# Performance work log

Hardware: AMD Instinct MI355X
Metric: run time of the kernel (lower is better)

The kernel has to match this reference:

```python
import jax, jax.numpy as jnp
import numpy as np

B, T, S, L, D, H = 2, 1024, 8, 256, 1024, 16
DH = D // H
EPS = 1e-5


def layer_norm(x, w, b):
    m = jnp.mean(x, axis=-1, keepdims=True)
    v = jnp.mean(jnp.square(x - m), axis=-1, keepdims=True)
    return (x - m) * jax.lax.rsqrt(v + EPS) * w + b


def setup_inputs() -> dict:
    key = jax.random.key(0)
    ks = jax.random.split(key, 12)
    s = 0.02
    return {
        "target_hidden": jax.random.normal(ks[0], (B, T, D), jnp.float32),
        "support_hidden": jax.random.normal(ks[1], (B, S, L, D), jnp.float32),
        "support_features": jax.random.normal(ks[2], (B, T, 3), jnp.float32),
        "support_token_mask": jax.random.randint(ks[3], (B, S, L), 0, 2).astype(bool),
        "ln_q_w": jnp.ones((D,), jnp.float32), "ln_q_b": jnp.zeros((D,), jnp.float32),
        "ln_kv_w": jnp.ones((D,), jnp.float32), "ln_kv_b": jnp.zeros((D,), jnp.float32),
        "out_ln_w": jnp.ones((D,), jnp.float32), "out_ln_b": jnp.zeros((D,), jnp.float32),
        "in_proj_w": jax.random.normal(ks[4], (3 * D, D), jnp.float32) * s,
        "in_proj_b": jnp.zeros((3 * D,), jnp.float32),
        "out_proj_w": jax.random.normal(ks[5], (D, D), jnp.float32) * s,
        "out_proj_b": jnp.zeros((D,), jnp.float32),
        "gate_w1": jax.random.normal(ks[6], (D, 2 * D + 3), jnp.float32) * s,
        "gate_b1": jnp.zeros((D,), jnp.float32),
        "gate_w2": jax.random.normal(ks[7], (1, D), jnp.float32) * s,
        "gate_b2": jnp.zeros((1,), jnp.float32),
    }


def _forward(target_hidden, support_hidden, support_features,
             ln_q_w, ln_q_b, ln_kv_w, ln_kv_b, out_ln_w, out_ln_b,
             in_proj_w, in_proj_b, out_proj_w, out_proj_b,
             gate_w1, gate_b1, gate_w2, gate_b2, support_token_mask):
    b, ns, sl, d = support_hidden.shape
    kv_len = ns * sl
    support_flat = support_hidden.reshape(b, kv_len, d)
    mask_flat = support_token_mask.reshape(b, kv_len)  # True = valid token

    q_in = layer_norm(target_hidden, ln_q_w, ln_q_b)
    kv_in = layer_norm(support_flat, ln_kv_w, ln_kv_b)

    # in-projection (torch MHA packed qkv weight)
    q = q_in @ in_proj_w[:d].T + in_proj_b[:d]
    k = kv_in @ in_proj_w[d:2 * d].T + in_proj_b[d:2 * d]
    v = kv_in @ in_proj_w[2 * d:].T + in_proj_b[2 * d:]

    qh = q.reshape(b, -1, H, DH)
    kh = k.reshape(b, kv_len, H, DH)
    vh = v.reshape(b, kv_len, H, DH)

    scores = jnp.einsum("bthd,bshd->bhts", qh, kh) / jnp.sqrt(jnp.float32(DH))
    scores = jnp.where(mask_flat[:, None, None, :], scores, -jnp.inf)
    probs = jax.nn.softmax(scores, axis=-1)
    ctx = jnp.einsum("bhts,bshd->bthd", probs, vh).reshape(b, -1, d)
    attn_out = ctx @ out_proj_w.T + out_proj_b

    gate_in = jnp.concatenate([target_hidden, attn_out, support_features], axis=-1)
    h = jax.nn.gelu(gate_in @ gate_w1.T + gate_b1, approximate=False)
    gate = jax.nn.sigmoid(h @ gate_w2.T + gate_b2)  # [b, t, 1]

    fused = gate * attn_out + (1.0 - gate) * target_hidden
    out = layer_norm(target_hidden + fused, out_ln_w, out_ln_b)
    return out, gate.squeeze(-1)


def reference(target_hidden, support_hidden, support_features, support_token_mask,
              ln_q_w, ln_q_b, ln_kv_w, ln_kv_b, out_ln_w, out_ln_b,
              in_proj_w, in_proj_b, out_proj_w, out_proj_b,
              gate_w1, gate_b1, gate_w2, gate_b2):
    return _forward(target_hidden, support_hidden, support_features,
                    ln_q_w, ln_q_b, ln_kv_w, ln_kv_b, out_ln_w, out_ln_b,
                    in_proj_w, in_proj_b, out_proj_w, out_proj_b,
                    gate_w1, gate_b1, gate_w2, gate_b2, support_token_mask)
```

## Files before the change

### kernel.cpp

```cpp
#include <hip/hip_runtime.h>
#include <stdint.h>

#define DEV __device__ __forceinline__

typedef __attribute__((ext_vector_type(8))) short bf16x8;
typedef __attribute__((ext_vector_type(4))) float f32x4;
typedef __attribute__((ext_vector_type(16))) float f32x16;
typedef __attribute__((ext_vector_type(8))) unsigned short ushort8;

DEV unsigned short f2bf(float f) {
  unsigned u = __float_as_uint(f);
  return (unsigned short)((u + 0x7fffu + ((u >> 16) & 1u)) >> 16);
}
DEV float bf2f(unsigned short h) { return __uint_as_float(((unsigned)h) << 16); }

DEV unsigned cvtpk(float lo, float hi) {
  unsigned r;
  asm("v_cvt_pk_bf16_f32 %0, %1, %2" : "=v"(r) : "v"(lo), "v"(hi));
  return r;
}
DEV void pl32swap(unsigned& a, unsigned& b) {
  asm volatile("v_permlane32_swap_b32 %0, %1" : "+v"(a), "+v"(b));
}

DEV void async16(const void* g, void* l) {
  __builtin_amdgcn_global_load_lds((const __attribute__((address_space(1))) void*)g,
                                   (__attribute__((address_space(3))) void*)l, 16, 0, 0);
}

__global__ void k_prep(const float4* __restrict__ ipw, const float4* __restrict__ opw,
                       const float* __restrict__ g1w, ushort4* __restrict__ Wbf,
                       ushort4* __restrict__ Wobf, unsigned short* __restrict__ Wg1bf) {
  int bid = blockIdx.x, t = threadIdx.x;
  if (bid < 3072) {
    int i = bid * 256 + t;
    float4 v = ipw[i];
    ushort4 o; o.x = f2bf(v.x); o.y = f2bf(v.y); o.z = f2bf(v.z); o.w = f2bf(v.w);
    Wbf[i] = o;
  } else if (bid < 4096) {
    int i = (bid - 3072) * 256 + t;
    float4 v = opw[i];
    ushort4 o; o.x = f2bf(v.x); o.y = f2bf(v.y); o.z = f2bf(v.z); o.w = f2bf(v.w);
    Wobf[i] = o;
  } else {
    for (int i = (bid - 4096) * 256 + t; i < 1024 * 2080; i += 2048 * 256) {
      int r = i / 2080, c = i - r * 2080;
      Wg1bf[i] = (c < 2051) ? f2bf(g1w[(size_t)r * 2051 + c]) : (unsigned short)0;
    }
  }
}

__global__ void k_mask_build(const unsigned char* __restrict__ m, unsigned short* __restrict__ mf) {
  int any = 0;
  for (int i = threadIdx.x; i < 4096; i += 256)
    if ((i & 3) != 0 && m[i] != 0) any = 1;
  unsigned long long ball = __ballot(any);
  __shared__ int sr[4];
  if ((threadIdx.x & 63) == 0) sr[threadIdx.x >> 6] = (ball != 0ULL) ? 1 : 0;
  __syncthreads();
  int isbool = sr[0] | sr[1] | sr[2] | sr[3];
  int i = blockIdx.x * 256 + threadIdx.x;
  if (i < 4096) {
    int v = isbool ? (m[i] != 0) : (((const int*)m)[i] != 0);
    mf[i] = v ? f2bf(-8.0f) : f2bf(-1e30f);
  }
}

__global__ void k_ln2(const float* __restrict__ tgt, const float* __restrict__ sup,
                      const float* __restrict__ qw, const float* __restrict__ qb,
                      const float* __restrict__ kw, const float* __restrict__ kb,
                      unsigned short* __restrict__ qin, unsigned short* __restrict__ kvin) {
  int row = blockIdx.x;
  const float *x, *w, *bb;
  unsigned short* y;
  if (row < 2048) { x = tgt + (size_t)row * 1024; w = qw; bb = qb; y = qin + (size_t)row * 1024; }
  else { int r = row - 2048; x = sup + (size_t)r * 1024; w = kw; bb = kb; y = kvin + (size_t)r * 1024; }
  float4 v = ((const float4*)x)[threadIdx.x];
  float s = v.x + v.y + v.z + v.w;
  float ss = v.x * v.x + v.y * v.y + v.z * v.z + v.w * v.w;
#pragma unroll
  for (int m = 32; m >= 1; m >>= 1) { s += __shfl_xor(s, m); ss += __shfl_xor(ss, m); }
  __shared__ float red[8];
  int wv = threadIdx.x >> 6;
  if ((threadIdx.x & 63) == 0) { red[wv] = s; red[4 + wv] = ss; }
  __syncthreads();
  s = red[0] + red[1] + red[2] + red[3];
  ss = red[4] + red[5] + red[6] + red[7];
  float mean = s * (1.f / 1024.f);
  float var = ss * (1.f / 1024.f) - mean * mean;
  float inv = rsqrtf(var + 1e-5f);
  float4 wv4 = ((const float4*)w)[threadIdx.x];
  float4 bv4 = ((const float4*)bb)[threadIdx.x];
  ushort4 o;
  o.x = f2bf((v.x - mean) * inv * wv4.x + bv4.x);
  o.y = f2bf((v.y - mean) * inv * wv4.y + bv4.y);
  o.z = f2bf((v.z - mean) * inv * wv4.z + bv4.z);
  o.w = f2bf((v.w - mean) * inv * wv4.w + bv4.w);
  ((ushort4*)y)[threadIdx.x] = o;
}

template <int BM, int BN, int OUTMODE>
DEV void gemm_body(const unsigned short* __restrict__ A, const unsigned short* __restrict__ B,
                   const float* __restrict__ bias, void* __restrict__ Cout, int N, int K,
                   int m0, int n0, float* __restrict__ aux, float oscale) {
  constexpr int WM = BM / 2, WN = BN / 2, FM = WM / 16, FN = WN / 16;
  __shared__ __align__(16) unsigned short As[2][BM * 32];
  __shared__ __align__(16) unsigned short Bs[2][BN * 32];
  int tid = threadIdx.x, l = tid & 63, w = tid >> 6;
  int wm = w >> 1, wn = w & 1;

  f32x4 acc[FM][FN];
#pragma unroll
  for (int m = 0; m < FM; m++)
#pragma unroll
    for (int n = 0; n < FN; n++) acc[m][n] = (f32x4){0.f, 0.f, 0.f, 0.f};

  auto stage = [&](int buf, int k0) {
#pragma unroll
    for (int i = 0; i < BM / 64; i++) {
      int r = i * 64 + w * 16 + (l >> 2);
      int cb = ((l & 3) * 16) ^ (((r >> 1) & 3) << 4);
      async16((const char*)A + (((size_t)(m0 + r) * K + k0) * 2 + cb),
              (char*)&As[buf][0] + (i * 64 + w * 16) * 64);
    }
#pragma unroll
    for (int i = 0; i < BN / 64; i++) {
      int r = i * 64 + w * 16 + (l >> 2);
      int cb = ((l & 3) * 16) ^ (((r >> 1) & 3) << 4);
      async16((const char*)B + (((size_t)(n0 + r) * K + k0) * 2 + cb),
              (char*)&Bs[buf][0] + (i * 64 + w * 16) * 64);
    }
  };

  int nk = K / 32;
  stage(0, 0);
  __syncthreads();
  int cur = 0;
  for (int kt = 0; kt < nk; kt++) {
    if (kt + 1 < nk) stage(cur ^ 1, (kt + 1) * 32);
    bf16x8 af[FM], bfr[FN];
#pragma unroll
    for (int m = 0; m < FM; m++) {
      int rr = wm * WM + m * 16 + (l & 15);
      af[m] = *(const bf16x8*)((const char*)&As[cur][0] + rr * 64 +
                               ((16 * (l >> 4)) ^ (((rr >> 1) & 3) << 4)));
    }
#pragma unroll
    for (int n = 0; n < FN; n++) {
      int rr = wn * WN + n * 16 + (l & 15);
      bfr[n] = *(const bf16x8*)((const char*)&Bs[cur][0] + rr * 64 +
                                ((16 * (l >> 4)) ^ (((rr >> 1) & 3) << 4)));
    }
    __builtin_amdgcn_s_setprio(1);
#pragma unroll
    for (int m = 0; m < FM; m++)
#pragma unroll
      for (int n = 0; n < FN; n++)
        acc[m][n] = __builtin_amdgcn_mfma_f32_16x16x32_bf16(af[m], bfr[n], acc[m][n], 0, 0, 0);
    __builtin_amdgcn_s_setprio(0);
    __syncthreads();
    cur ^= 1;
  }

#pragma unroll
  for (int m = 0; m < FM; m++)
#pragma unroll
    for (int n = 0; n < FN; n++)
#pragma unroll
      for (int r = 0; r < 4; r++) {
        int gr = m0 + wm * WM + m * 16 + (l >> 4) * 4 + r;
        int gc = n0 + wn * WN + n * 16 + (l & 15);
        float v = (acc[m][n][r] + bias[gc]) * oscale;
        if (OUTMODE == 2) v = 0.5f * v * (1.f + erff(v * 0.70710678118f));
        if (OUTMODE == 3) {
          aux[(size_t)gr * 1024 + gc] = v;
          ((unsigned short*)Cout)[(size_t)gr * 2080 + 1024 + gc] = f2bf(v);
        } else {
          ((unsigned short*)Cout)[(size_t)gr * N + gc] = f2bf(v);
        }
      }
}

template <int BM, int BN, int OUTMODE>
__global__ __launch_bounds__(256, 2)
void k_gemm(const unsigned short* __restrict__ A, const unsigned short* __restrict__ B,
            const float* __restrict__ bias, void* __restrict__ Cout, int N, int K,
            int nx, float* __restrict__ aux) {
  int cpx = gridDim.x >> 3;
  int orig = (blockIdx.x & 7) * cpx + (blockIdx.x >> 3);
  int m0 = (orig / nx) * BM, n0 = (orig % nx) * BN;
  gemm_body<BM, BN, OUTMODE>(A, B, bias, Cout, N, K, m0, n0, aux, 1.0f);
}

__global__ __launch_bounds__(256, 2)
void k_inproj(const unsigned short* __restrict__ qin, const unsigned short* __restrict__ kvin,
              const unsigned short* __restrict__ Wbf, const float* __restrict__ ipb,
              unsigned short* __restrict__ qbuf, unsigned short* __restrict__ kvbuf) {
  int cpx = gridDim.x >> 3;
  int orig = (blockIdx.x & 7) * cpx + (blockIdx.x >> 3);
  if (orig < 128) {
    int m0 = (orig >> 3) * 128, n0 = (orig & 7) * 128;
    gemm_body<128, 128, 0>(qin, Wbf, ipb, qbuf, 1024, 1024, m0, n0, nullptr, 0.125f);
  } else {
    int t = orig - 128;
    int m0 = (t >> 4) * 128, n0 = (t & 15) * 128;
    gemm_body<128, 128, 0>(kvin, Wbf + 1024 * 1024, ipb + 1024, kvbuf, 2048, 1024, m0, n0,
                           nullptr, 1.0f);
  }
}

__global__ void k_transpose_v(const unsigned short* __restrict__ kvb,
                              unsigned short* __restrict__ vt) {
  __shared__ unsigned short t[64][66];
  int kv0 = blockIdx.x * 64, d0 = blockIdx.y * 64, b = blockIdx.z;
  for (int i = threadIdx.x; i < 4096; i += 256) {
    int r = i >> 6, c = i & 63;
    t[r][c] = kvb[(size_t)(b * 2048 + kv0 + r) * 2048 + 1024 + d0 + c];
  }
  __syncthreads();
  for (int i = threadIdx.x; i < 4096; i += 256) {
    int r = i >> 6, c = i & 63;
    vt[(size_t)(b * 1024 + d0 + r) * 2048 + kv0 + c] = t[c][r];
  }
}

__global__ __launch_bounds__(256, 2)
void k_attn(const unsigned short* __restrict__ qb, const unsigned short* __restrict__ kvb,
            const unsigned short* __restrict__ vt, const unsigned short* __restrict__ maskbf,
            unsigned short* __restrict__ pot, float* __restrict__ plsum) {
  __shared__ __align__(16) unsigned short Kt[2][32 * 64];
  __shared__ __align__(16) unsigned short Vt[2][64 * 32];
  __shared__ __align__(16) unsigned short mls[512];
  int tid = threadIdx.x, l = tid & 63, w = tid >> 6;
  int hi = l >> 5, q32 = l & 31;
  int id = blockIdx.x;
  int hb = id & 31, rest = id >> 5;
  int qt = rest >> 2, seg = rest & 3;
  int h = hb & 15, b = hb >> 4;
  int qrow = qt * 128 + w * 32 + q32;
  int kv0base = seg * 512;

  bf16x8 fq[4];
  const char* qsrc = (const char*)qb + (((size_t)(b * 1024 + qrow)) * 1024 + h * 64 + hi * 8) * 2;
#pragma unroll
  for (int i = 0; i < 4; i++) fq[i] = *(const bf16x8*)(qsrc + i * 32);

  bf16x8 onesB = {0, 0, 0, 0, 0, 0, 0, 0};
  if (hi == 0) onesB[0] = (short)0x3F80;

  f32x16 oa0 = {0, 0, 0, 0, 0, 0, 0, 0, 0, 0, 0, 0, 0, 0, 0, 0};
  f32x16 oa1 = {0, 0, 0, 0, 0, 0, 0, 0, 0, 0, 0, 0, 0, 0, 0, 0};
  float plocal = 0.f;

  if (w == 0)
    async16((const char*)maskbf + ((size_t)b * 2048 + kv0base) * 2 + l * 16, (char*)mls);

  const char* kgb = (const char*)kvb + ((size_t)(b * 2048)) * 4096 + h * 128;
  const char* vgb = (const char*)vt + ((size_t)(b * 1024 + h * 64)) * 4096;
  int kcb = (((l & 7) ^ ((l >> 3) & 7)) << 4);
  int vcb = (((l & 3) ^ ((l >> 3) & 3)) << 4);

  auto stage = [&](int buf, int kv0) {
    async16(kgb + (size_t)(kv0 + w * 8 + (l >> 3)) * 4096 + kcb, (char*)&Kt[buf][0] + w * 1024);
    async16(vgb + (size_t)(w * 16 + (l >> 2)) * 4096 + (size_t)kv0 * 2 + vcb,
            (char*)&Vt[buf][0] + w * 1024);
  };

  stage(0, kv0base);
  __syncthreads();
  int cur = 0;

  int kfs = q32 & 7;
  int vfs = (q32 >> 1) & 3;

  for (int t = 0; t < 16; t++) {
    int kv0 = kv0base + t * 32;
    if (t < 15) stage(cur ^ 1, kv0 + 32);

    f32x16 sac = {0, 0, 0, 0, 0, 0, 0, 0, 0, 0, 0, 0, 0, 0, 0, 0};
    const char* kt = (const char*)&Kt[cur][0];
    __builtin_amdgcn_s_setprio(1);
#pragma unroll
    for (int i = 0; i < 4; i++) {
      bf16x8 ka = *(const bf16x8*)(kt + q32 * 128 + (((i * 2 + hi) ^ kfs) << 4));
      sac = __builtin_amdgcn_mfma_f32_32x32x16_bf16(ka, fq[i], sac, 0, 0, 0);
    }
    unsigned short mv = mls[t * 32 + q32];
    bf16x8 ma = {0, 0, 0, 0, 0, 0, 0, 0};
    if (hi == 0) ma[0] = (short)mv;
    sac = __builtin_amdgcn_mfma_f32_32x32x16_bf16(ma, onesB, sac, 0, 0, 0);
    __builtin_amdgcn_s_setprio(0);

    float p[16];
#pragma unroll
    for (int j = 0; j < 16; j++) p[j] = __expf(sac[j]);
#pragma unroll
    for (int j = 0; j < 16; j++) plocal += p[j];

    bf16x8 pf[2];
#pragma unroll
    for (int c = 0; c < 2; c++) {
      unsigned A0 = cvtpk(p[c * 8 + 0], p[c * 8 + 1]);
      unsigned A1 = cvtpk(p[c * 8 + 2], p[c * 8 + 3]);
      unsigned B0 = cvtpk(p[c * 8 + 4], p[c * 8 + 5]);
      unsigned B1 = cvtpk(p[c * 8 + 6], p[c * 8 + 7]);
      pl32swap(A0, B0);
      pl32swap(A1, B1);
      unsigned fr[4] = {A0, A1, B0, B1};
      pf[c] = *(const bf16x8*)fr;
    }

    const char* vtb = (const char*)&Vt[cur][0];
    __builtin_amdgcn_s_setprio(1);
#pragma unroll
    for (int c = 0; c < 2; c++) {
      bf16x8 va0 = *(const bf16x8*)(vtb + q32 * 64 + (((c * 2 + hi) ^ vfs) << 4));
      bf16x8 va1 = *(const bf16x8*)(vtb + (32 + q32) * 64 + (((c * 2 + hi) ^ vfs) << 4));
      oa0 = __builtin_amdgcn_mfma_f32_32x32x16_bf16(va0, pf[c], oa0, 0, 0, 0);
      oa1 = __builtin_amdgcn_mfma_f32_32x32x16_bf16(va1, pf[c], oa1, 0, 0, 0);
    }
    __builtin_amdgcn_s_setprio(0);
    __syncthreads();
    cur ^= 1;
  }

  float ptot = plocal + __shfl_xor(plocal, 32);
  if (hi == 0) plsum[((size_t)seg * 2048 + b * 1024 + qrow) * 16 + h] = ptot;

  size_t pb = (((size_t)seg * 2 + b) * 16 + h) * 64;
#pragma unroll
  for (int j = 0; j < 16; j++) {
    int d0 = (j & 3) + 8 * (j >> 2) + 4 * hi;
    pot[(pb + d0) * 1024 + qrow] = f2bf(oa0[j]);
    pot[(pb + 32 + d0) * 1024 + qrow] = f2bf(oa1[j]);
  }
}

__global__ void k_combine_t(const unsigned short* __restrict__ pot,
                            const float* __restrict__ plsum, unsigned short* __restrict__ ctx) {
  __shared__ float sinv[64];
  __shared__ __align__(16) unsigned short tl[64][72];
  int t = threadIdx.x;
  int id = blockIdx.x;
  int qt2 = id & 15, bh = id >> 4, h = bh & 15, b = bh >> 4;
  int q0 = qt2 * 64;

  if (t < 64) {
    float s = 0.f;
#pragma unroll
    for (int seg = 0; seg < 4; seg++)
      s += plsum[((size_t)seg * 2048 + b * 1024 + q0 + t) * 16 + h];
    sinv[t] = 1.f / s;
  }

  int d = t >> 2, qo = (t & 3) * 16;
  float acc[16];
#pragma unroll
  for (int j = 0; j < 16; j++) acc[j] = 0.f;
#pragma unroll
  for (int seg = 0; seg < 4; seg++) {
    size_t base = ((((size_t)seg * 2 + b) * 16 + h) * 64 + d) * 1024 + q0 + qo;
    ushort8 v0 = *(const ushort8*)(pot + base);
    ushort8 v1 = *(const ushort8*)(pot + base + 8);
#pragma unroll
    for (int j = 0; j < 8; j++) { acc[j] += bf2f(v0[j]); acc[8 + j] += bf2f(v1[j]); }
  }
  __syncthreads();
#pragma unroll
  for (int j = 0; j < 16; j++) tl[qo + j][d] = f2bf(acc[j] * sinv[qo + j]);
  __syncthreads();

  int q = t >> 2, dof = (t & 3) * 16;
  ushort8 a = *(const ushort8*)&tl[q][dof];
  ushort8 c8 = *(const ushort8*)&tl[q][dof + 8];
  size_t ob = ((size_t)(b * 1024 + q0 + q)) * 1024 + h * 64 + dof;
  *(ushort8*)(ctx + ob) = a;
  *(ushort8*)(ctx + ob + 8) = c8;
}

__global__ void k_gin_static(const float* __restrict__ target, const float* __restrict__ feats,
                             unsigned short* __restrict__ gi) {
  int i = blockIdx.x * 256 + threadIdx.x;
  const int ntgt = 2048 * 1024;
  if (i < ntgt) {
    int r = i >> 10, c = i & 1023;
    gi[(size_t)r * 2080 + c] = f2bf(target[i]);
  } else {
    int j = i - ntgt;
    if (j < 2048 * 32) {
      int r = j >> 5, c = j & 31;
      gi[(size_t)r * 2080 + 2048 + c] = (c < 3) ? f2bf(feats[r * 3 + c]) : (unsigned short)0;
    }
  }
}

__global__ void k_gatefinal(const unsigned short* __restrict__ hm, const float* __restrict__ w2,
                            const float* __restrict__ b2, const float* __restrict__ target,
                            const float* __restrict__ attn, const float* __restrict__ w,
                            const float* __restrict__ bb, float* __restrict__ out,
                            float* __restrict__ gout) {
  int row = blockIdx.x;
  float4 w2v = ((const float4*)w2)[threadIdx.x];
  ushort4 hv = ((const ushort4*)(hm + (size_t)row * 1024))[threadIdx.x];
  float s = bf2f(hv.x) * w2v.x + bf2f(hv.y) * w2v.y + bf2f(hv.z) * w2v.z + bf2f(hv.w) * w2v.w;
#pragma unroll
  for (int m = 32; m >= 1; m >>= 1) s += __shfl_xor(s, m);
  __shared__ float red[8];
  __shared__ float gsh;
  if ((threadIdx.x & 63) == 0) red[threadIdx.x >> 6] = s;
  __syncthreads();
  if (threadIdx.x == 0) {
    float tt = red[0] + red[1] + red[2] + red[3] + b2[0];
    float gv = 1.f / (1.f + __expf(-tt));
    gsh = gv;
    gout[row] = gv;
  }
  __syncthreads();
  float gv = gsh;

  float4 t = ((const float4*)(target + (size_t)row * 1024))[threadIdx.x];
  float4 a = ((const float4*)(attn + (size_t)row * 1024))[threadIdx.x];
  float4 y;
  y.x = (2.f - gv) * t.x + gv * a.x;
  y.y = (2.f - gv) * t.y + gv * a.y;
  y.z = (2.f - gv) * t.z + gv * a.z;
  y.w = (2.f - gv) * t.w + gv * a.w;
  float sm = y.x + y.y + y.z + y.w;
  float ss = y.x * y.x + y.y * y.y + y.z * y.z + y.w * y.w;
#pragma unroll
  for (int m = 32; m >= 1; m >>= 1) { sm += __shfl_xor(sm, m); ss += __shfl_xor(ss, m); }
  if ((threadIdx.x & 63) == 0) { red[threadIdx.x >> 6] = sm; red[4 + (threadIdx.x >> 6)] = ss; }
  __syncthreads();
  sm = red[0] + red[1] + red[2] + red[3];
  ss = red[4] + red[5] + red[6] + red[7];
  float mean = sm * (1.f / 1024.f);
  float var = ss * (1.f / 1024.f) - mean * mean;
  float inv = rsqrtf(var + 1e-5f);
  float4 wv4 = ((const float4*)w)[threadIdx.x];
  float4 bv4 = ((const float4*)bb)[threadIdx.x];
  float4 o;
  o.x = (y.x - mean) * inv * wv4.x + bv4.x;
  o.y = (y.y - mean) * inv * wv4.y + bv4.y;
  o.z = (y.z - mean) * inv * wv4.z + bv4.z;
  o.w = (y.w - mean) * inv * wv4.w + bv4.w;
  ((float4*)(out + (size_t)row * 1024))[threadIdx.x] = o;
}

extern "C" void kernel_launch(void* const* d_in, const int* in_sizes, int n_in,
                              void* d_out, int out_size, void* d_ws, size_t ws_size,
                              hipStream_t stream) {
  const float* target     = (const float*)d_in[0];
  const float* support    = (const float*)d_in[1];
  const float* feats      = (const float*)d_in[2];
  const void*  maskp      = d_in[3];
  const float* ln_q_w     = (const float*)d_in[4];
  const float* ln_q_b     = (const float*)d_in[5];
  const float* ln_kv_w    = (const float*)d_in[6];
  const float* ln_kv_b    = (const float*)d_in[7];
  const float* out_ln_w   = (const float*)d_in[8];
  const float* out_ln_b   = (const float*)d_in[9];
  const float* in_proj_w  = (const float*)d_in[10];
  const float* in_proj_b  = (const float*)d_in[11];
  const float* out_proj_w = (const float*)d_in[12];
  const float* out_proj_b = (const float*)d_in[13];
  const float* gate_w1    = (const float*)d_in[14];
  const float* gate_b1    = (const float*)d_in[15];
  const float* gate_w2    = (const float*)d_in[16];
  const float* gate_b2    = (const float*)d_in[17];

  if (ws_size < 84615168ULL) return;

  char* ws = (char*)d_ws;
  unsigned short* Wbf    = (unsigned short*)(ws + 0);
  unsigned short* Wobf   = (unsigned short*)(ws + 6291456);
  unsigned short* Wg1bf  = (unsigned short*)(ws + 8388608);
  unsigned short* qin    = (unsigned short*)(ws + 12648448);
  unsigned short* kvin   = (unsigned short*)(ws + 16842752);
  unsigned short* qbuf   = (unsigned short*)(ws + 25231360);
  unsigned short* kvbuf  = (unsigned short*)(ws + 29425664);
  unsigned short* vtbuf  = (unsigned short*)(ws + 12648448);
  unsigned short* hbuf   = (unsigned short*)(ws + 25231360);
  unsigned short* ctx    = (unsigned short*)(ws + 46202880);
  float*          attn   = (float*)(ws + 50397184);
  unsigned short* gin    = (unsigned short*)(ws + 58785792);
  unsigned short* pot    = (unsigned short*)(ws + 67305472);
  float*          plsum  = (float*)(ws + 84082688);
  unsigned short* maskbf = (unsigned short*)(ws + 84606976);

  float* outp = (float*)d_out;

  k_mask_build<<<16, 256, 0, stream>>>((const unsigned char*)maskp, maskbf);
  k_prep<<<6144, 256, 0, stream>>>((const float4*)in_proj_w, (const float4*)out_proj_w,
                                   gate_w1, (ushort4*)Wbf, (ushort4*)Wobf, Wg1bf);
  k_gin_static<<<(2048 * 1056 + 255) / 256, 256, 0, stream>>>(target, feats, gin);
  k_ln2<<<6144, 256, 0, stream>>>(target, support, ln_q_w, ln_q_b, ln_kv_w, ln_kv_b, qin, kvin);

  k_inproj<<<640, 256, 0, stream>>>(qin, kvin, Wbf, in_proj_b, qbuf, kvbuf);
  k_transpose_v<<<dim3(32, 16, 2), 256, 0, stream>>>(kvbuf, vtbuf);

  k_attn<<<1024, 256, 0, stream>>>(qbuf, kvbuf, vtbuf, maskbf, pot, plsum);
  k_combine_t<<<512, 256, 0, stream>>>(pot, plsum, ctx);

  k_gemm<64, 64, 3><<<512, 256, 0, stream>>>(ctx, Wobf, out_proj_b, gin, 1024, 1024, 16, attn);

  k_gemm<64, 64, 2><<<512, 256, 0, stream>>>(gin, Wg1bf, gate_b1, hbuf, 1024, 2080, 16, nullptr);

  k_gatefinal<<<2048, 256, 0, stream>>>(hbuf, gate_w2, gate_b2, target, attn,
                                        out_ln_w, out_ln_b, outp, outp + 2 * 1024 * 1024);
}
```

Measured before the change: 265.9 us.

## Fold out-projection into gate weights and merge prep launches into one kernel

The attention branch of the gate's first layer is rewritten algebraically. The gate weights for that branch are pre-multiplied by the transposed out-projection weights, giving a matrix F and a folded bias, so one post-attention GEMM against [Wo; F] produces both attn_out and its gate contribution. The target/features part of the gate GEMM and the F product move into the in-projection launch, and the separate mask, prep, gin and layernorm kernels are merged into one big prep launch. This is meant to shorten the serial chain after attention and cut launch count. In exchange it adds an extra 1024^3 GEMM per call, a larger workspace, and extra bf16 rounding from computing F in reduced precision.

```diff
diff --git a/kernel.cpp b/kernel.cpp
--- a/kernel.cpp
+++ b/kernel.cpp
@@ -28,84 +28,135 @@
                                    (__attribute__((address_space(3))) void*)l, 16, 0, 0);
 }
 
-__global__ void k_prep(const float4* __restrict__ ipw, const float4* __restrict__ opw,
-                       const float* __restrict__ g1w, ushort4* __restrict__ Wbf,
-                       ushort4* __restrict__ Wobf, unsigned short* __restrict__ Wg1bf) {
+__global__ void k_prep_all(const unsigned char* __restrict__ mask, const float4* __restrict__ ipw,
+                           const float* __restrict__ opw, const float* __restrict__ g1w,
+                           const float* __restrict__ tgt, const float* __restrict__ feats,
+                           const float* __restrict__ sup,
+                           const float* __restrict__ qw, const float* __restrict__ qb,
+                           const float* __restrict__ kw, const float* __restrict__ kb,
+                           const float* __restrict__ bo,
+                           unsigned short* __restrict__ maskbf, ushort4* __restrict__ Wbf,
+                           unsigned short* __restrict__ Wobf, unsigned short* __restrict__ WoT,
+                           unsigned short* __restrict__ Wg1attn, unsigned short* __restrict__ Wg1ab,
+                           unsigned short* __restrict__ tgtfeats, unsigned short* __restrict__ qin,
+                           unsigned short* __restrict__ kvin, float* __restrict__ pbias) {
+  __shared__ unsigned short tl[64][65];
+  __shared__ float red[8];
+  __shared__ int sr[4];
   int bid = blockIdx.x, t = threadIdx.x;
-  if (bid < 3072) {
+  if (bid < 16) {
+    int any = 0;
+    for (int i = t; i < 4096; i += 256)
+      if ((i & 3) != 0 && mask[i] != 0) any = 1;
+    unsigned long long ball = __ballot(any);
+    if ((t & 63) == 0) sr[t >> 6] = (ball != 0ULL) ? 1 : 0;
+    __syncthreads();
+    int isbool = sr[0] | sr[1] | sr[2] | sr[3];
     int i = bid * 256 + t;
+    int v = isbool ? (mask[i] != 0) : (((const int*)mask)[i] != 0);
+    maskbf[i] = v ? f2bf(-8.0f) : f2bf(-1e30f);
+  } else if (bid < 3088) {
+    int i = (bid - 16) * 256 + t;
     float4 v = ipw[i];
     ushort4 o; o.x = f2bf(v.x); o.y = f2bf(v.y); o.z = f2bf(v.z); o.w = f2bf(v.w);
     Wbf[i] = o;
-  } else if (bid < 4096) {
-    int i = (bid - 3072) * 256 + t;
-    float4 v = opw[i];
-    ushort4 o; o.x = f2bf(v.x); o.y = f2bf(v.y); o.z = f2bf(v.z); o.w = f2bf(v.w);
-    Wobf[i] = o;
+  } else if (bid < 3344) {
+    int b2 = bid - 3088;
+    int r0 = (b2 >> 4) * 64, c0 = (b2 & 15) * 64;
+#pragma unroll
+    for (int i = 0; i < 16; i++) {
+      int idx = i * 256 + t, rr = idx >> 6, cc = idx & 63;
+      unsigned short bv = f2bf(opw[(size_t)(r0 + rr) * 1024 + c0 + cc]);
+      Wobf[(size_t)(r0 + rr) * 1024 + c0 + cc] = bv;
+      tl[cc][rr] = bv;
+    }
+    __syncthreads();
+#pragma unroll
+    for (int i = 0; i < 16; i++) {
+      int idx = i * 256 + t, rr = idx & 63, cc = idx >> 6;
+      WoT[(size_t)(c0 + cc) * 1024 + r0 + rr] = tl[cc][rr];
+    }
+  } else if (bid < 4368) {
+    int r = bid - 3344;
+    const float* src = g1w + (size_t)r * 2051 + 1024;
+    int c = t * 4;
+    ushort4 o;
+    o.x = f2bf(src[c]); o.y = f2bf(src[c + 1]); o.z = f2bf(src[c + 2]); o.w = f2bf(src[c + 3]);
+    *(ushort4*)(Wg1attn + (size_t)r * 1024 + c) = o;
+  } else if (bid < 5392) {
+    int r = bid - 4368;
+    const float* src = g1w + (size_t)r * 2051;
+    for (int q = t; q < 264; q += 256) {
+      int c = q * 4;
+      ushort4 o;
+#pragma unroll
+      for (int j = 0; j < 4; j++) {
+        int cs = c + j;
+        float v = (cs < 1024) ? src[cs] : ((cs < 1027) ? src[1024 + cs] : 0.f);
+        ((unsigned short*)&o)[j] = f2bf(v);
+      }
+      *(ushort4*)(Wg1ab + (size_t)r * 1056 + c) = o;
+    }
+  } else if (bid < 7440) {
+    int r = bid - 5392;
+    for (int q = t; q < 264; q += 256) {
+      int c = q * 4;
+      ushort4 o;
+#pragma unroll
+      for (int j = 0; j < 4; j++) {
+        int cs = c + j;
+        float v = (cs < 1024) ? tgt[(size_t)r * 1024 + cs]
+                              : ((cs < 1027) ? feats[r * 3 + cs - 1024] : 0.f);
+        ((unsigned short*)&o)[j] = f2bf(v);
+      }
+      *(ushort4*)(tgtfeats + (size_t)r * 1056 + c) = o;
+    }
+  } else if (bid < 13584) {
+    int row = bid - 7440;
+    const float *x, *w, *bb2;
+    unsigned short* y;
+    if (row < 2048) { x = tgt + (size_t)row * 1024; w = qw; bb2 = qb; y = qin + (size_t)row * 1024; }
+    else { int r = row - 2048; x = sup + (size_t)r * 1024; w = kw; bb2 = kb; y = kvin + (size_t)r * 1024; }
+    float4 v = ((const float4*)x)[t];
+    float s = v.x + v.y + v.z + v.w;
+    float ss = v.x * v.x + v.y * v.y + v.z * v.z + v.w * v.w;
+#pragma unroll
+    for (int m = 32; m >= 1; m >>= 1) { s += __shfl_xor(s, m); ss += __shfl_xor(ss, m); }
+    int wv = t >> 6;
+    if ((t & 63) == 0) { red[wv] = s; red[4 + wv] = ss; }
+    __syncthreads();
+    s = red[0] + red[1] + red[2] + red[3];
+    ss = red[4] + red[5] + red[6] + red[7];
+    float mean = s * (1.f / 1024.f);
+    float var = ss * (1.f / 1024.f) - mean * mean;
+    float inv = rsqrtf(var + 1e-5f);
+    float4 wv4 = ((const float4*)w)[t];
+    float4 bv4 = ((const float4*)bb2)[t];
+    ushort4 o;
+    o.x = f2bf((v.x - mean) * inv * wv4.x + bv4.x);
+    o.y = f2bf((v.y - mean) * inv * wv4.y + bv4.y);
+    o.z = f2bf((v.z - mean) * inv * wv4.z + bv4.z);
+    o.w = f2bf((v.w - mean) * inv * wv4.w + bv4.w);
+    ((ushort4*)y)[t] = o;
+  } else if (bid < 13648) {
+    int b7 = bid - 13584;
+    int n = b7 * 16 + (t >> 4), l16 = t & 15;
+    const float* wrow = g1w + (size_t)n * 2051 + 1024;
+    float s = 0.f;
+    for (int j = 0; j < 64; j++) s += bo[l16 + 16 * j] * wrow[l16 + 16 * j];
+#pragma unroll
+    for (int m = 1; m < 16; m <<= 1) s += __shfl_xor(s, m);
+    if (l16 == 0) pbias[1024 + n] = s;
   } else {
-    for (int i = (bid - 4096) * 256 + t; i < 1024 * 2080; i += 2048 * 256) {
-      int r = i / 2080, c = i - r * 2080;
-      Wg1bf[i] = (c < 2051) ? f2bf(g1w[(size_t)r * 2051 + c]) : (unsigned short)0;
-    }
-  }
-}
-
-__global__ void k_mask_build(const unsigned char* __restrict__ m, unsigned short* __restrict__ mf) {
-  int any = 0;
-  for (int i = threadIdx.x; i < 4096; i += 256)
-    if ((i & 3) != 0 && m[i] != 0) any = 1;
-  unsigned long long ball = __ballot(any);
-  __shared__ int sr[4];
-  if ((threadIdx.x & 63) == 0) sr[threadIdx.x >> 6] = (ball != 0ULL) ? 1 : 0;
-  __syncthreads();
-  int isbool = sr[0] | sr[1] | sr[2] | sr[3];
-  int i = blockIdx.x * 256 + threadIdx.x;
-  if (i < 4096) {
-    int v = isbool ? (m[i] != 0) : (((const int*)m)[i] != 0);
-    mf[i] = v ? f2bf(-8.0f) : f2bf(-1e30f);
-  }
-}
-
-__global__ void k_ln2(const float* __restrict__ tgt, const float* __restrict__ sup,
-                      const float* __restrict__ qw, const float* __restrict__ qb,
-                      const float* __restrict__ kw, const float* __restrict__ kb,
-                      unsigned short* __restrict__ qin, unsigned short* __restrict__ kvin) {
-  int row = blockIdx.x;
-  const float *x, *w, *bb;
-  unsigned short* y;
-  if (row < 2048) { x = tgt + (size_t)row * 1024; w = qw; bb = qb; y = qin + (size_t)row * 1024; }
-  else { int r = row - 2048; x = sup + (size_t)r * 1024; w = kw; bb = kb; y = kvin + (size_t)r * 1024; }
-  float4 v = ((const float4*)x)[threadIdx.x];
-  float s = v.x + v.y + v.z + v.w;
-  float ss = v.x * v.x + v.y * v.y + v.z * v.z + v.w * v.w;
-#pragma unroll
-  for (int m = 32; m >= 1; m >>= 1) { s += __shfl_xor(s, m); ss += __shfl_xor(ss, m); }
-  __shared__ float red[8];
-  int wv = threadIdx.x >> 6;
-  if ((threadIdx.x & 63) == 0) { red[wv] = s; red[4 + wv] = ss; }
-  __syncthreads();
-  s = red[0] + red[1] + red[2] + red[3];
-  ss = red[4] + red[5] + red[6] + red[7];
-  float mean = s * (1.f / 1024.f);
-  float var = ss * (1.f / 1024.f) - mean * mean;
-  float inv = rsqrtf(var + 1e-5f);
-  float4 wv4 = ((const float4*)w)[threadIdx.x];
-  float4 bv4 = ((const float4*)bb)[threadIdx.x];
-  ushort4 o;
-  o.x = f2bf((v.x - mean) * inv * wv4.x + bv4.x);
-  o.y = f2bf((v.y - mean) * inv * wv4.y + bv4.y);
-  o.z = f2bf((v.z - mean) * inv * wv4.z + bv4.z);
-  o.w = f2bf((v.w - mean) * inv * wv4.w + bv4.w);
-  ((ushort4*)y)[threadIdx.x] = o;
+    ((float4*)pbias)[t] = ((const float4*)bo)[t];
+  }
 }
 
 template <int BM, int BN, int OUTMODE>
 DEV void gemm_body(const unsigned short* __restrict__ A, const unsigned short* __restrict__ B,
                    const float* __restrict__ bias, void* __restrict__ Cout, int N, int K,
-                   int m0, int n0, float* __restrict__ aux, float oscale) {
+                   int m0, int n0, float oscale, unsigned short* As, unsigned short* Bs) {
   constexpr int WM = BM / 2, WN = BN / 2, FM = WM / 16, FN = WN / 16;
-  __shared__ __align__(16) unsigned short As[2][BM * 32];
-  __shared__ __align__(16) unsigned short Bs[2][BN * 32];
   int tid = threadIdx.x, l = tid & 63, w = tid >> 6;
   int wm = w >> 1, wn = w & 1;
 
@@ -121,14 +172,14 @@
       int r = i * 64 + w * 16 + (l >> 2);
       int cb = ((l & 3) * 16) ^ (((r >> 1) & 3) << 4);
       async16((const char*)A + (((size_t)(m0 + r) * K + k0) * 2 + cb),
-              (char*)&As[buf][0] + (i * 64 + w * 16) * 64);
+              (char*)As + buf * (BM * 64) + (i * 64 + w * 16) * 64);
     }
 #pragma unroll
     for (int i = 0; i < BN / 64; i++) {
       int r = i * 64 + w * 16 + (l >> 2);
       int cb = ((l & 3) * 16) ^ (((r >> 1) & 3) << 4);
       async16((const char*)B + (((size_t)(n0 + r) * K + k0) * 2 + cb),
-              (char*)&Bs[buf][0] + (i * 64 + w * 16) * 64);
+              (char*)Bs + buf * (BN * 64) + (i * 64 + w * 16) * 64);
     }
   };
 
@@ -142,13 +193,13 @@
 #pragma unroll
     for (int m = 0; m < FM; m++) {
       int rr = wm * WM + m * 16 + (l & 15);
-      af[m] = *(const bf16x8*)((const char*)&As[cur][0] + rr * 64 +
+      af[m] = *(const bf16x8*)((const char*)As + cur * (BM * 64) + rr * 64 +
                                ((16 * (l >> 4)) ^ (((rr >> 1) & 3) << 4)));
     }
 #pragma unroll
     for (int n = 0; n < FN; n++) {
       int rr = wn * WN + n * 16 + (l & 15);
-      bfr[n] = *(const bf16x8*)((const char*)&Bs[cur][0] + rr * 64 +
+      bfr[n] = *(const bf16x8*)((const char*)Bs + cur * (BN * 64) + rr * 64 +
                                 ((16 * (l >> 4)) ^ (((rr >> 1) & 3) << 4)));
     }
     __builtin_amdgcn_s_setprio(1);
@@ -170,43 +221,55 @@
       for (int r = 0; r < 4; r++) {
         int gr = m0 + wm * WM + m * 16 + (l >> 4) * 4 + r;
         int gc = n0 + wn * WN + n * 16 + (l & 15);
-        float v = (acc[m][n][r] + bias[gc]) * oscale;
-        if (OUTMODE == 2) v = 0.5f * v * (1.f + erff(v * 0.70710678118f));
-        if (OUTMODE == 3) {
-          aux[(size_t)gr * 1024 + gc] = v;
-          ((unsigned short*)Cout)[(size_t)gr * 2080 + 1024 + gc] = f2bf(v);
-        } else {
+        float v = acc[m][n][r];
+        if (OUTMODE != 4) v += bias[gc];
+        v *= oscale;
+        if (OUTMODE == 1)
+          ((float*)Cout)[(size_t)gr * N + gc] = v;
+        else
           ((unsigned short*)Cout)[(size_t)gr * N + gc] = f2bf(v);
-        }
       }
 }
 
-template <int BM, int BN, int OUTMODE>
 __global__ __launch_bounds__(256, 2)
-void k_gemm(const unsigned short* __restrict__ A, const unsigned short* __restrict__ B,
-            const float* __restrict__ bias, void* __restrict__ Cout, int N, int K,
-            int nx, float* __restrict__ aux) {
-  int cpx = gridDim.x >> 3;
-  int orig = (blockIdx.x & 7) * cpx + (blockIdx.x >> 3);
-  int m0 = (orig / nx) * BM, n0 = (orig % nx) * BN;
-  gemm_body<BM, BN, OUTMODE>(A, B, bias, Cout, N, K, m0, n0, aux, 1.0f);
-}
-
-__global__ __launch_bounds__(256, 2)
-void k_inproj(const unsigned short* __restrict__ qin, const unsigned short* __restrict__ kvin,
-              const unsigned short* __restrict__ Wbf, const float* __restrict__ ipb,
-              unsigned short* __restrict__ qbuf, unsigned short* __restrict__ kvbuf) {
+void k_mm1(const unsigned short* __restrict__ qin, const unsigned short* __restrict__ kvin,
+           const unsigned short* __restrict__ tgtfeats, const unsigned short* __restrict__ Wg1attn,
+           const unsigned short* __restrict__ Wbf, const unsigned short* __restrict__ Wg1ab,
+           const unsigned short* __restrict__ WoT, const float* __restrict__ ipb,
+           const float* __restrict__ g1b, unsigned short* __restrict__ qbuf,
+           unsigned short* __restrict__ kvbuf, float* __restrict__ h1buf,
+           unsigned short* __restrict__ Fbf) {
+  __shared__ __align__(16) unsigned short As[2 * 128 * 32];
+  __shared__ __align__(16) unsigned short Bs[2 * 128 * 32];
   int cpx = gridDim.x >> 3;
   int orig = (blockIdx.x & 7) * cpx + (blockIdx.x >> 3);
   if (orig < 128) {
-    int m0 = (orig >> 3) * 128, n0 = (orig & 7) * 128;
-    gemm_body<128, 128, 0>(qin, Wbf, ipb, qbuf, 1024, 1024, m0, n0, nullptr, 0.125f);
+    gemm_body<128, 128, 0>(qin, Wbf, ipb, qbuf, 1024, 1024, (orig >> 3) * 128, (orig & 7) * 128,
+                           0.125f, As, Bs);
+  } else if (orig < 640) {
+    int t = orig - 128;
+    gemm_body<128, 128, 0>(kvin, Wbf + 1024 * 1024, ipb + 1024, kvbuf, 2048, 1024,
+                           (t >> 4) * 128, (t & 15) * 128, 1.0f, As, Bs);
+  } else if (orig < 768) {
+    int t = orig - 640;
+    gemm_body<128, 128, 1>(tgtfeats, Wg1ab, g1b, h1buf, 1024, 1056, (t >> 3) * 128,
+                           (t & 7) * 128, 1.0f, As, Bs);
   } else {
-    int t = orig - 128;
-    int m0 = (t >> 4) * 128, n0 = (t & 15) * 128;
-    gemm_body<128, 128, 0>(kvin, Wbf + 1024 * 1024, ipb + 1024, kvbuf, 2048, 1024, m0, n0,
-                           nullptr, 1.0f);
-  }
+    int t = orig - 768;
+    gemm_body<64, 64, 4>(Wg1attn, WoT, nullptr, Fbf, 1024, 1024, (t >> 4) * 64, (t & 15) * 64,
+                         1.0f, As, Bs);
+  }
+}
+
+__global__ __launch_bounds__(256, 2)
+void k_mm2(const unsigned short* __restrict__ ctx, const unsigned short* __restrict__ Bw,
+           const float* __restrict__ pbias, float* __restrict__ hc) {
+  __shared__ __align__(16) unsigned short As[2 * 128 * 32];
+  __shared__ __align__(16) unsigned short Bs[2 * 64 * 32];
+  int cpx = gridDim.x >> 3;
+  int orig = (blockIdx.x & 7) * cpx + (blockIdx.x >> 3);
+  gemm_body<128, 64, 1>(ctx, Bw, pbias, hc, 2048, 1024, (orig >> 5) * 128, (orig & 31) * 64,
+                        1.0f, As, Bs);
 }
 
 __global__ void k_transpose_v(const unsigned short* __restrict__ kvb,
@@ -378,38 +441,29 @@
   *(ushort8*)(ctx + ob + 8) = c8;
 }
 
-__global__ void k_gin_static(const float* __restrict__ target, const float* __restrict__ feats,
-                             unsigned short* __restrict__ gi) {
-  int i = blockIdx.x * 256 + threadIdx.x;
-  const int ntgt = 2048 * 1024;
-  if (i < ntgt) {
-    int r = i >> 10, c = i & 1023;
-    gi[(size_t)r * 2080 + c] = f2bf(target[i]);
-  } else {
-    int j = i - ntgt;
-    if (j < 2048 * 32) {
-      int r = j >> 5, c = j & 31;
-      gi[(size_t)r * 2080 + 2048 + c] = (c < 3) ? f2bf(feats[r * 3 + c]) : (unsigned short)0;
-    }
-  }
-}
-
-__global__ void k_gatefinal(const unsigned short* __restrict__ hm, const float* __restrict__ w2,
-                            const float* __restrict__ b2, const float* __restrict__ target,
-                            const float* __restrict__ attn, const float* __restrict__ w,
+__global__ void k_gatefinal(const float* __restrict__ h1, const float* __restrict__ hc,
+                            const float* __restrict__ w2, const float* __restrict__ b2,
+                            const float* __restrict__ target, const float* __restrict__ w,
                             const float* __restrict__ bb, float* __restrict__ out,
                             float* __restrict__ gout) {
-  int row = blockIdx.x;
-  float4 w2v = ((const float4*)w2)[threadIdx.x];
-  ushort4 hv = ((const ushort4*)(hm + (size_t)row * 1024))[threadIdx.x];
-  float s = bf2f(hv.x) * w2v.x + bf2f(hv.y) * w2v.y + bf2f(hv.z) * w2v.z + bf2f(hv.w) * w2v.w;
+  int row = blockIdx.x, t = threadIdx.x;
+  float4 h1v = ((const float4*)(h1 + (size_t)row * 1024))[t];
+  float4 hav = ((const float4*)(hc + (size_t)row * 2048 + 1024))[t];
+  float4 w2v = ((const float4*)w2)[t];
+  float4 g4;
+  g4.x = h1v.x + hav.x; g4.y = h1v.y + hav.y; g4.z = h1v.z + hav.z; g4.w = h1v.w + hav.w;
+  g4.x = 0.5f * g4.x * (1.f + erff(g4.x * 0.70710678118f));
+  g4.y = 0.5f * g4.y * (1.f + erff(g4.y * 0.70710678118f));
+  g4.z = 0.5f * g4.z * (1.f + erff(g4.z * 0.70710678118f));
+  g4.w = 0.5f * g4.w * (1.f + erff(g4.w * 0.70710678118f));
+  float s = g4.x * w2v.x + g4.y * w2v.y + g4.z * w2v.z + g4.w * w2v.w;
 #pragma unroll
   for (int m = 32; m >= 1; m >>= 1) s += __shfl_xor(s, m);
   __shared__ float red[8];
   __shared__ float gsh;
-  if ((threadIdx.x & 63) == 0) red[threadIdx.x >> 6] = s;
-  __syncthreads();
-  if (threadIdx.x == 0) {
+  if ((t & 63) == 0) red[t >> 6] = s;
+  __syncthreads();
+  if (t == 0) {
     float tt = red[0] + red[1] + red[2] + red[3] + b2[0];
     float gv = 1.f / (1.f + __expf(-tt));
     gsh = gv;
@@ -418,32 +472,32 @@
   __syncthreads();
   float gv = gsh;
 
-  float4 t = ((const float4*)(target + (size_t)row * 1024))[threadIdx.x];
-  float4 a = ((const float4*)(attn + (size_t)row * 1024))[threadIdx.x];
+  float4 tg = ((const float4*)(target + (size_t)row * 1024))[t];
+  float4 a = ((const float4*)(hc + (size_t)row * 2048))[t];
   float4 y;
-  y.x = (2.f - gv) * t.x + gv * a.x;
-  y.y = (2.f - gv) * t.y + gv * a.y;
-  y.z = (2.f - gv) * t.z + gv * a.z;
-  y.w = (2.f - gv) * t.w + gv * a.w;
+  y.x = (2.f - gv) * tg.x + gv * a.x;
+  y.y = (2.f - gv) * tg.y + gv * a.y;
+  y.z = (2.f - gv) * tg.z + gv * a.z;
+  y.w = (2.f - gv) * tg.w + gv * a.w;
   float sm = y.x + y.y + y.z + y.w;
   float ss = y.x * y.x + y.y * y.y + y.z * y.z + y.w * y.w;
 #pragma unroll
   for (int m = 32; m >= 1; m >>= 1) { sm += __shfl_xor(sm, m); ss += __shfl_xor(ss, m); }
-  if ((threadIdx.x & 63) == 0) { red[threadIdx.x >> 6] = sm; red[4 + (threadIdx.x >> 6)] = ss; }
+  if ((t & 63) == 0) { red[t >> 6] = sm; red[4 + (t >> 6)] = ss; }
   __syncthreads();
   sm = red[0] + red[1] + red[2] + red[3];
   ss = red[4] + red[5] + red[6] + red[7];
   float mean = sm * (1.f / 1024.f);
   float var = ss * (1.f / 1024.f) - mean * mean;
   float inv = rsqrtf(var + 1e-5f);
-  float4 wv4 = ((const float4*)w)[threadIdx.x];
-  float4 bv4 = ((const float4*)bb)[threadIdx.x];
+  float4 wv4 = ((const float4*)w)[t];
+  float4 bv4 = ((const float4*)bb)[t];
   float4 o;
   o.x = (y.x - mean) * inv * wv4.x + bv4.x;
   o.y = (y.y - mean) * inv * wv4.y + bv4.y;
   o.z = (y.z - mean) * inv * wv4.z + bv4.z;
   o.w = (y.w - mean) * inv * wv4.w + bv4.w;
-  ((float4*)(out + (size_t)row * 1024))[threadIdx.x] = o;
+  ((float4*)(out + (size_t)row * 1024))[t] = o;
 }
 
 extern "C" void kernel_launch(void* const* d_in, const int* in_sizes, int n_in,
@@ -468,43 +522,47 @@
   const float* gate_w2    = (const float*)d_in[16];
   const float* gate_b2    = (const float*)d_in[17];
 
-  if (ws_size < 84615168ULL) return;
+  if (ws_size < 109789184ULL) return;
 
   char* ws = (char*)d_ws;
-  unsigned short* Wbf    = (unsigned short*)(ws + 0);
-  unsigned short* Wobf   = (unsigned short*)(ws + 6291456);
-  unsigned short* Wg1bf  = (unsigned short*)(ws + 8388608);
-  unsigned short* qin    = (unsigned short*)(ws + 12648448);
-  unsigned short* kvin   = (unsigned short*)(ws + 16842752);
-  unsigned short* qbuf   = (unsigned short*)(ws + 25231360);
-  unsigned short* kvbuf  = (unsigned short*)(ws + 29425664);
-  unsigned short* vtbuf  = (unsigned short*)(ws + 12648448);
-  unsigned short* hbuf   = (unsigned short*)(ws + 25231360);
-  unsigned short* ctx    = (unsigned short*)(ws + 46202880);
-  float*          attn   = (float*)(ws + 50397184);
-  unsigned short* gin    = (unsigned short*)(ws + 58785792);
-  unsigned short* pot    = (unsigned short*)(ws + 67305472);
-  float*          plsum  = (float*)(ws + 84082688);
-  unsigned short* maskbf = (unsigned short*)(ws + 84606976);
+  unsigned short* Wbf      = (unsigned short*)(ws + 0);
+  unsigned short* Wobf     = (unsigned short*)(ws + 6291456);
+  unsigned short* Fbf      = (unsigned short*)(ws + 8388608);
+  unsigned short* WoT      = (unsigned short*)(ws + 10485760);
+  unsigned short* Wg1attn  = (unsigned short*)(ws + 12582912);
+  unsigned short* Wg1ab    = (unsigned short*)(ws + 14680064);
+  unsigned short* tgtfeats = (unsigned short*)(ws + 16842752);
+  unsigned short* qin      = (unsigned short*)(ws + 21168128);
+  unsigned short* kvin     = (unsigned short*)(ws + 25362432);
+  unsigned short* qbuf     = (unsigned short*)(ws + 33751040);
+  unsigned short* kvbuf    = (unsigned short*)(ws + 37945344);
+  unsigned short* vtbuf    = (unsigned short*)(ws + 54722560);
+  float*          h1buf    = (float*)(ws + 63111168);
+  unsigned short* pot      = (unsigned short*)(ws + 71499776);
+  float*          plsum    = (float*)(ws + 88276992);
+  unsigned short* ctx      = (unsigned short*)(ws + 88801280);
+  float*          hc       = (float*)(ws + 92995584);
+  float*          pbias    = (float*)(ws + 109772800);
+  unsigned short* maskbf   = (unsigned short*)(ws + 109780992);
 
   float* outp = (float*)d_out;
 
-  k_mask_build<<<16, 256, 0, stream>>>((const unsigned char*)maskp, maskbf);
-  k_prep<<<6144, 256, 0, stream>>>((const float4*)in_proj_w, (const float4*)out_proj_w,
-                                   gate_w1, (ushort4*)Wbf, (ushort4*)Wobf, Wg1bf);
-  k_gin_static<<<(2048 * 1056 + 255) / 256, 256, 0, stream>>>(target, feats, gin);
-  k_ln2<<<6144, 256, 0, stream>>>(target, support, ln_q_w, ln_q_b, ln_kv_w, ln_kv_b, qin, kvin);
-
-  k_inproj<<<640, 256, 0, stream>>>(qin, kvin, Wbf, in_proj_b, qbuf, kvbuf);
+  k_prep_all<<<13649, 256, 0, stream>>>((const unsigned char*)maskp, (const float4*)in_proj_w,
+                                        out_proj_w, gate_w1, target, feats, support,
+                                        ln_q_w, ln_q_b, ln_kv_w, ln_kv_b, out_proj_b,
+                                        maskbf, (ushort4*)Wbf, Wobf, WoT, Wg1attn, Wg1ab,
+                                        tgtfeats, qin, kvin, pbias);
+
+  k_mm1<<<1024, 256, 0, stream>>>(qin, kvin, tgtfeats, Wg1attn, Wbf, Wg1ab, WoT,
+                                  in_proj_b, gate_b1, qbuf, kvbuf, h1buf, Fbf);
+
   k_transpose_v<<<dim3(32, 16, 2), 256, 0, stream>>>(kvbuf, vtbuf);
 
   k_attn<<<1024, 256, 0, stream>>>(qbuf, kvbuf, vtbuf, maskbf, pot, plsum);
   k_combine_t<<<512, 256, 0, stream>>>(pot, plsum, ctx);
 
-  k_gemm<64, 64, 3><<<512, 256, 0, stream>>>(ctx, Wobf, out_proj_b, gin, 1024, 1024, 16, attn);
-
-  k_gemm<64, 64, 2><<<512, 256, 0, stream>>>(gin, Wg1bf, gate_b1, hbuf, 1024, 2080, 16, nullptr);
-
-  k_gatefinal<<<2048, 256, 0, stream>>>(hbuf, gate_w2, gate_b2, target, attn,
+  k_mm2<<<512, 256, 0, stream>>>(ctx, Wobf, pbias, hc);
+
+  k_gatefinal<<<2048, 256, 0, stream>>>(h1buf, hc, gate_w2, gate_b2, target,
                                         out_ln_w, out_ln_b, outp, outp + 2 * 1024 * 1024);
 }
```

After: 238.1 us. 1.12x faster.
